# Optimization experiments

Hardware: AMD Instinct MI355X
Metric: run time of the kernel (lower is better)

The kernel has to match this reference:

```python
import jax, jax.numpy as jnp
import numpy as np

EPS = 1e-5

def setup_inputs() -> dict:
    key = jax.random.key(0)
    ks = jax.random.split(key, 12)
    N, d0, d1, d2, qh, qo = 8192, 128, 256, 256, 128, 1
    state = jax.random.normal(ks[0], (N, d0), dtype=jnp.float32)
    adjacent_matrix = jax.random.uniform(ks[1], (N, N), dtype=jnp.float32)
    s = 0.05
    return {
        "state": state,
        "adjacent_matrix": adjacent_matrix,
        "gamma": jnp.ones((d0,), jnp.float32),
        "beta": jnp.zeros((d0,), jnp.float32),
        "W1": jax.random.normal(ks[2], (d0, d1), jnp.float32) * s,
        "b1": jnp.zeros((d1,), jnp.float32),
        "W2": jax.random.normal(ks[3], (d1, d2), jnp.float32) * s,
        "b2": jnp.zeros((d2,), jnp.float32),
        "Wq1": jax.random.normal(ks[4], (d2, qh), jnp.float32) * s,
        "bq1": jnp.zeros((qh,), jnp.float32),
        "Wq2": jax.random.normal(ks[5], (qh, qo), jnp.float32) * s,
        "bq2": jnp.zeros((qo,), jnp.float32),
    }


def reference(state, adjacent_matrix, gamma, beta, W1, b1, W2, b2, Wq1, bq1, Wq2, bq2):
    # LinkBatchNorm: BatchNorm1d over node (batch) axis, training-mode statistics
    mean = jnp.mean(state, axis=0)
    var = jnp.var(state, axis=0)
    x = (state - mean) * jax.lax.rsqrt(var + EPS) * gamma + beta  # [N, d0]
    # GraphCNN: two layers of relu(A @ X @ W + b)
    h = jax.nn.relu(adjacent_matrix @ (x @ W1) + b1)   # [N, d1]
    h = jax.nn.relu(adjacent_matrix @ (h @ W2) + b2)   # [N, d2]
    # QNetwork: per-node MLP -> Q value
    q = jax.nn.relu(h @ Wq1 + bq1) @ Wq2 + bq2         # [N, 1]
    return q
```

## Files before the change

kernel.cpp:

```cpp
#include <hip/hip_runtime.h>
#include <stdint.h>

#define NN 8192
#define D0 128
#define D1 256
#define D2 256
#define QH 128
#define EPSV 1e-5f

using bf16x8 = __attribute__((ext_vector_type(8))) __bf16;
using f32x4  = __attribute__((ext_vector_type(4))) float;

__device__ __forceinline__ unsigned short f2bf(float f) {
    union { float f; unsigned int u; } v; v.f = f;
    unsigned int r = v.u + 0x7FFFu + ((v.u >> 16) & 1u);
    return (unsigned short)(r >> 16);
}
__device__ __forceinline__ float bf2f(unsigned short h) {
    union { unsigned int u; float f; } v; v.u = ((unsigned int)h) << 16;
    return v.f;
}
__device__ __forceinline__ void async_ld16(const void* g, void* l) {
    __builtin_amdgcn_global_load_lds(
        (__attribute__((address_space(1))) void*)(g),
        (__attribute__((address_space(3))) void*)(l), 16, 0, 0);
}

__global__ __launch_bounds__(256) void k_castA(const float* __restrict__ A,
                                               unsigned short* __restrict__ Abf,
                                               float* __restrict__ rs) {
    __shared__ float sred[256];
    int t = threadIdx.x;
    size_t row = blockIdx.x;
    const float* ap = A + row * NN;
    unsigned short* op = Abf + row * NN;
    float s = 0.f;
#pragma unroll
    for (int i = 0; i < 8; ++i) {
        int c = i * 1024 + t * 4;
        float4 v = *(const float4*)(ap + c);
        s += v.x + v.y + v.z + v.w;
        ushort4 o; o.x = f2bf(v.x); o.y = f2bf(v.y); o.z = f2bf(v.z); o.w = f2bf(v.w);
        *(ushort4*)(op + c) = o;
    }
    sred[t] = s;
    __syncthreads();
    if (t < 128) sred[t] += sred[t + 128];
    __syncthreads();
    if (t < 64) {
        float v = sred[t] + sred[t + 64];
#pragma unroll
        for (int d = 32; d > 0; d >>= 1) v += __shfl_down(v, d, 64);
        if (t == 0) rs[row] = v;
    }
}

__global__ void k_zero(float* __restrict__ p) {
    p[blockIdx.x * 256 + threadIdx.x] = 0.f;
}

__global__ void k_stats(const float* __restrict__ state,
                        float* __restrict__ psum, float* __restrict__ psq) {
    int j = threadIdx.x;
    int b = blockIdx.x;
    const float* p = state + (size_t)b * 32 * D0 + j;
    float s = 0.f, sq = 0.f;
#pragma unroll 4
    for (int r = 0; r < 32; ++r) { float x = p[(size_t)r * D0]; s += x; sq += x * x; }
    psum[b * D0 + j] = s;
    psq [b * D0 + j] = sq;
}

__global__ void k_finalize(const float* __restrict__ psum, const float* __restrict__ psq,
                           const float* __restrict__ gamma, const float* __restrict__ beta,
                           const float* __restrict__ W1,
                           float* __restrict__ scale, float* __restrict__ shift,
                           float* __restrict__ c1) {
    __shared__ float s_shift[D0];
    int t = threadIdx.x;
    if (t < D0) {
        float s = 0.f, sq = 0.f;
        for (int b = 0; b < 256; ++b) { s += psum[b * D0 + t]; sq += psq[b * D0 + t]; }
        float mean = s * (1.0f / NN);
        float var  = sq * (1.0f / NN) - mean * mean;
        float sc = gamma[t] * rsqrtf(var + EPSV);
        float sh = beta[t] - mean * sc;
        scale[t] = sc; shift[t] = sh; s_shift[t] = sh;
    }
    __syncthreads();
    float acc = 0.f;
    for (int k = 0; k < D0; ++k) acc += s_shift[k] * W1[(size_t)k * D1 + t];
    c1[t] = acc;
}

__global__ void k_prep_weights(const float* __restrict__ W1, const float* __restrict__ W2,
                               const float* __restrict__ scale,
                               unsigned short* __restrict__ W1st,
                               unsigned short* __restrict__ W2t) {
    int idx = blockIdx.x * 256 + threadIdx.x;
    if (idx < 32768) {
        int n = idx >> 7, k = idx & 127;
        W1st[idx] = f2bf(W1[(size_t)k * D1 + n] * scale[k]);
    } else {
        int i = idx - 32768; int n = i >> 8, k = i & 255;
        W2t[i] = f2bf(W2[(size_t)k * D2 + n]);
    }
}

template <int N, int K, bool A_FP32, bool BIAS>
__global__ __launch_bounds__(256, 4) void k_small_gemm(
        const void* __restrict__ Aptr, const unsigned short* __restrict__ Bt,
        const float* __restrict__ bias, unsigned short* __restrict__ out) {
    constexpr int WN = N / 4;
    constexpr int NJ = WN / 16;
    constexpr int BI = N / 64;
    __shared__ unsigned short Alds[32 * 32];
    __shared__ unsigned short Blds[N * 32];
    int t = threadIdx.x, lane = t & 63, w = t >> 6;
    int m0 = blockIdx.x * 32;
    int lr = lane & 15, lk = (lane >> 4) * 8;
    int wc = w * WN;
    f32x4 acc[2][NJ] = {};

    for (int kk = 0; kk < K; kk += 32) {
        __syncthreads();
        if constexpr (A_FP32) {
            const float* A = (const float*)Aptr;
            int row = t >> 3, kc = (t & 7) * 4;
            float4 v = *(const float4*)(A + (size_t)(m0 + row) * K + kk + kc);
            uint2 p;
            p.x = ((unsigned)f2bf(v.y) << 16) | f2bf(v.x);
            p.y = ((unsigned)f2bf(v.w) << 16) | f2bf(v.z);
            *(uint2*)&Alds[row * 32 + kc] = p;
        } else {
            if (w < 2) {
                const unsigned short* A = (const unsigned short*)Aptr;
                int row = w * 16 + (lane >> 2);
                async_ld16(A + (size_t)(m0 + row) * K + kk + (lane & 3) * 8, &Alds[w * 512]);
            }
        }
#pragma unroll
        for (int i = 0; i < BI; ++i) {
            int n = w * WN + i * 16 + (lane >> 2);
            async_ld16(Bt + (size_t)n * K + kk + (lane & 3) * 8, &Blds[(w * WN + i * 16) * 32]);
        }
        __syncthreads();
        bf16x8 a[2], b[NJ];
#pragma unroll
        for (int i = 0; i < 2; ++i) a[i] = *(const bf16x8*)&Alds[(i * 16 + lr) * 32 + lk];
#pragma unroll
        for (int j = 0; j < NJ; ++j) b[j] = *(const bf16x8*)&Blds[(wc + j * 16 + lr) * 32 + lk];
#pragma unroll
        for (int i = 0; i < 2; ++i)
#pragma unroll
            for (int j = 0; j < NJ; ++j)
                acc[i][j] = __builtin_amdgcn_mfma_f32_16x16x32_bf16(a[i], b[j], acc[i][j], 0, 0, 0);
    }
    int q = lane >> 4;
#pragma unroll
    for (int j = 0; j < NJ; ++j) {
        int n = wc + j * 16 + lr;
        float bv = 0.f;
        if constexpr (BIAS) bv = bias[n];
#pragma unroll
        for (int i = 0; i < 2; ++i) {
#pragma unroll
            for (int r = 0; r < 4; ++r) {
                int m = m0 + i * 16 + q * 4 + r;
                out[(size_t)m * N + n] = f2bf(acc[i][j][r] + bv);
            }
        }
    }
}

__global__ void k_transpose(const unsigned short* __restrict__ in, unsigned short* __restrict__ out,
                            float* __restrict__ colsum) {
    __shared__ unsigned short tile[64 * 68];
    __shared__ float cp[4][64];
    int t = threadIdx.x;
    int r0 = blockIdx.x * 64, c0 = blockIdx.y * 64;
#pragma unroll
    for (int p = 0; p < 4; ++p) {
        int row = (t >> 4) + p * 16, col = (t & 15) * 4;
        *(ushort4*)&tile[row * 68 + col] = *(const ushort4*)&in[(size_t)(r0 + row) * 256 + c0 + col];
    }
    __syncthreads();
    int n = t >> 2;
#pragma unroll
    for (int s = 0; s < 2; ++s) {
        int mo = (t & 3) * 16 + s * 8;
        unsigned short v[8];
#pragma unroll
        for (int e = 0; e < 8; ++e) v[e] = tile[(mo + e) * 68 + n];
        *(uint4*)&out[(size_t)(c0 + n) * NN + r0 + mo] = *(const uint4*)v;
    }
    int col = t & 63, gg = t >> 6;
    float s = 0.f;
#pragma unroll
    for (int r = 0; r < 16; ++r) s += bf2f(tile[(gg * 16 + r) * 68 + col]);
    cp[gg][col] = s;
    __syncthreads();
    if (t < 64) atomicAdd(colsum + c0 + t, cp[0][t] + cp[1][t] + cp[2][t] + cp[3][t]);
}

__global__ __launch_bounds__(512, 4) void k_big_gemm2(
        const unsigned short* __restrict__ Abf, const unsigned short* __restrict__ Yt,
        float* __restrict__ Cp) {
    __shared__ unsigned short Alds[128 * 32];
    __shared__ unsigned short Blds[256 * 32];
    int t = threadIdx.x, lane = t & 63, w = t >> 6;
    int m0 = blockIdx.x * 128;
    int kbeg = blockIdx.y * 1024;
    int wr = (w & 1) * 64, wc = (w >> 1) * 64;
    int lr = lane & 15, q = lane >> 4;
    f32x4 acc[4][4] = {};

    int srow = lane >> 2;
    int hsw = (lane & 3) ^ ((srow ^ (srow >> 2)) & 3);
    const unsigned short* agp = Abf + (size_t)(m0 + w * 16 + srow) * NN + kbeg + hsw * 8;
    const unsigned short* bg0 = Yt + (size_t)(w * 32 + srow) * NN + kbeg + hsw * 8;
    const unsigned short* bg1 = Yt + (size_t)(w * 32 + 16 + srow) * NN + kbeg + hsw * 8;
    unsigned short* aLb = Alds + w * 512;
    unsigned short* bLb0 = Blds + w * 1024;
    unsigned short* bLb1 = Blds + w * 1024 + 512;
    int xsr = (lr ^ (lr >> 2)) & 3;
    int lks = ((q ^ xsr) & 3) * 8;

    for (int kk = 0; kk < 1024; kk += 32) {
        __syncthreads();
        async_ld16(agp + kk, aLb);
        async_ld16(bg0 + kk, bLb0);
        async_ld16(bg1 + kk, bLb1);
        __syncthreads();
        bf16x8 a[4], b[4];
#pragma unroll
        for (int i = 0; i < 4; ++i) a[i] = *(const bf16x8*)&Alds[(wr + i * 16 + lr) * 32 + lks];
#pragma unroll
        for (int j = 0; j < 4; ++j) b[j] = *(const bf16x8*)&Blds[(wc + j * 16 + lr) * 32 + lks];
#pragma unroll
        for (int i = 0; i < 4; ++i)
#pragma unroll
            for (int j = 0; j < 4; ++j)
                acc[i][j] = __builtin_amdgcn_mfma_f32_16x16x32_bf16(a[i], b[j], acc[i][j], 0, 0, 0);
    }
    float* outp = Cp + (size_t)blockIdx.y * NN * 256;
#pragma unroll
    for (int i = 0; i < 4; ++i)
#pragma unroll
        for (int j = 0; j < 4; ++j) {
            int n = wc + j * 16 + lr;
#pragma unroll
            for (int r = 0; r < 4; ++r) {
                int m = m0 + wr + i * 16 + q * 4 + r;
                outp[(size_t)m * 256 + n] = acc[i][j][r];
            }
        }
}

__global__ void k_s2(const float* __restrict__ colB, const float* __restrict__ colH1,
                     const float* __restrict__ W2, float* __restrict__ s2) {
    int n = threadIdx.x;
    float acc = 0.f;
    for (int k = 0; k < 256; ++k) acc += colH1[k] * W2[(size_t)k * 256 + n];
    s2[n] = colB[n] - acc;
}

__global__ __launch_bounds__(256) void k_reduce8(
        const float* __restrict__ Cp, const float* __restrict__ rsA,
        const float* __restrict__ bias, const float* __restrict__ sn,
        unsigned short* __restrict__ out, float* __restrict__ colH1) {
    __shared__ float rs_s[16];
    __shared__ float cs[4][256];
    int t = threadIdx.x;
    int m0 = blockIdx.x * 16;
    const size_t S = (size_t)NN * 256;
    if (t < 16) rs_s[t] = rsA[m0 + t] * (1.0f / 8192.0f);
    __syncthreads();
    int g = t >> 6, cq = (t & 63) * 4;
    float4 snv = *(const float4*)(sn + cq);
    float4 bv  = *(const float4*)(bias + cq);
    float c0 = 0.f, c1a = 0.f, c2 = 0.f, c3 = 0.f;
#pragma unroll
    for (int r4 = 0; r4 < 4; ++r4) {
        int row = g * 4 + r4;
        size_t base = (size_t)(m0 + row) * 256 + cq;
        float4 a = {0.f, 0.f, 0.f, 0.f};
#pragma unroll
        for (int s = 0; s < 8; ++s) {
            float4 p = *(const float4*)(Cp + (size_t)s * S + base);
            a.x += p.x; a.y += p.y; a.z += p.z; a.w += p.w;
        }
        float rsv = rs_s[row];
        float x0 = fmaxf(a.x + bv.x - rsv * snv.x, 0.f);
        float x1 = fmaxf(a.y + bv.y - rsv * snv.y, 0.f);
        float x2 = fmaxf(a.z + bv.z - rsv * snv.z, 0.f);
        float x3 = fmaxf(a.w + bv.w - rsv * snv.w, 0.f);
        ushort4 o; o.x = f2bf(x0); o.y = f2bf(x1); o.z = f2bf(x2); o.w = f2bf(x3);
        *(ushort4*)(out + base) = o;
        c0 += x0; c1a += x1; c2 += x2; c3 += x3;
    }
    cs[g][cq] = c0; cs[g][cq + 1] = c1a; cs[g][cq + 2] = c2; cs[g][cq + 3] = c3;
    __syncthreads();
    float tot = cs[0][t] + cs[1][t] + cs[2][t] + cs[3][t];
    atomicAdd(colH1 + t, tot);
}

__global__ __launch_bounds__(256) void k_reduce_qhead(
        const float* __restrict__ Cp, const float* __restrict__ rsA,
        const float* __restrict__ bias, const float* __restrict__ sn,
        const float* __restrict__ Wq1, const float* __restrict__ bq1,
        const float* __restrict__ Wq2, const float* __restrict__ bq2,
        float* __restrict__ out) {
    __shared__ float sh[16][256];
    __shared__ float rs_s[16];
    __shared__ float red[4][8];
    int t = threadIdx.x;
    int m0 = blockIdx.x * 16;
    const size_t S = (size_t)NN * 256;
    if (t < 16) rs_s[t] = rsA[m0 + t] * (1.0f / 8192.0f);
    __syncthreads();
    int g = t >> 6, cq = (t & 63) * 4;
    float4 snv = *(const float4*)(sn + cq);
    float4 bv  = *(const float4*)(bias + cq);
#pragma unroll
    for (int r4 = 0; r4 < 4; ++r4) {
        int row = g * 4 + r4;
        size_t base = (size_t)(m0 + row) * 256 + cq;
        float4 a = {0.f, 0.f, 0.f, 0.f};
#pragma unroll
        for (int s = 0; s < 8; ++s) {
            float4 p = *(const float4*)(Cp + (size_t)s * S + base);
            a.x += p.x; a.y += p.y; a.z += p.z; a.w += p.w;
        }
        float rsv = rs_s[row];
        float4 o;
        o.x = fmaxf(a.x + bv.x - rsv * snv.x, 0.f);
        o.y = fmaxf(a.y + bv.y - rsv * snv.y, 0.f);
        o.z = fmaxf(a.z + bv.z - rsv * snv.z, 0.f);
        o.w = fmaxf(a.w + bv.w - rsv * snv.w, 0.f);
        *(float4*)&sh[row][cq] = o;
    }
    __syncthreads();
    int h = t & 127, rg = t >> 7;
    float acc[8] = {};
    for (int n = 0; n < 256; ++n) {
        float wv = Wq1[(size_t)n * QH + h];
#pragma unroll
        for (int r = 0; r < 8; ++r) acc[r] = fmaf(sh[rg * 8 + r][n], wv, acc[r]);
    }
    float b1v = bq1[h], w2v = Wq2[h];
    int wid = t >> 6, lane = t & 63;
#pragma unroll
    for (int r = 0; r < 8; ++r) {
        float v = fmaxf(acc[r] + b1v, 0.f) * w2v;
#pragma unroll
        for (int d = 32; d > 0; d >>= 1) v += __shfl_down(v, d, 64);
        if (lane == 0) red[wid][r] = v;
    }
    __syncthreads();
    if (t < 16) {
        int rg2 = t >> 3, r = t & 7;
        out[m0 + rg2 * 8 + r] = red[rg2 * 2][r] + red[rg2 * 2 + 1][r] + bq2[0];
    }
}

extern "C" void kernel_launch(void* const* d_in, const int* in_sizes, int n_in,
                              void* d_out, int out_size, void* d_ws, size_t ws_size,
                              hipStream_t stream) {
    const float* state = (const float*)d_in[0];
    const float* adj   = (const float*)d_in[1];
    const float* gamma = (const float*)d_in[2];
    const float* beta  = (const float*)d_in[3];
    const float* W1    = (const float*)d_in[4];
    const float* b1    = (const float*)d_in[5];
    const float* W2    = (const float*)d_in[6];
    const float* b2    = (const float*)d_in[7];
    const float* Wq1   = (const float*)d_in[8];
    const float* bq1   = (const float*)d_in[9];
    const float* Wq2   = (const float*)d_in[10];
    const float* bq2   = (const float*)d_in[11];
    float* out = (float*)d_out;

    char* ws = (char*)d_ws;
    float* psum  = (float*)(ws + 0);
    float* psq   = (float*)(ws + 131072);
    float* scale = (float*)(ws + 262144);
    float* shift = (float*)(ws + 262656);
    float* c1    = (float*)(ws + 263168);
    float* colA  = (float*)(ws + 264192);
    float* colB  = (float*)(ws + 265216);
    float* colH1 = (float*)(ws + 266240);
    float* s2    = (float*)(ws + 267264);
    unsigned short* W1st = (unsigned short*)(ws + 268288);
    unsigned short* W2t  = (unsigned short*)(ws + 333824);
    unsigned short* Ybuf = (unsigned short*)(ws + (size_t)1  * (1u << 20));
    unsigned short* Ytb  = (unsigned short*)(ws + (size_t)5  * (1u << 20));
    unsigned short* Hbuf = (unsigned short*)(ws + (size_t)9  * (1u << 20));
    float*          rsA  = (float*)(ws + (size_t)14 * (1u << 20));
    float*          Cp   = (float*)(ws + (size_t)22 * (1u << 20));
    unsigned short* Abf  = (unsigned short*)(ws + (size_t)128 * (1u << 20));

    k_castA<<<8192, 256, 0, stream>>>(adj, Abf, rsA);
    k_zero<<<4, 256, 0, stream>>>(colA);
    k_stats<<<256, 128, 0, stream>>>(state, psum, psq);
    k_finalize<<<1, 256, 0, stream>>>(psum, psq, gamma, beta, W1, scale, shift, c1);
    k_prep_weights<<<384, 256, 0, stream>>>(W1, W2, scale, W1st, W2t);

    k_small_gemm<256, 128, true, true><<<256, 256, 0, stream>>>(state, W1st, c1, Ybuf);
    k_transpose<<<dim3(128, 4), 256, 0, stream>>>(Ybuf, Ytb, colA);
    k_big_gemm2<<<dim3(64, 8), 512, 0, stream>>>(Abf, Ytb, Cp);
    k_reduce8<<<512, 256, 0, stream>>>(Cp, rsA, b1, colA, Hbuf, colH1);

    k_small_gemm<256, 256, false, false><<<256, 256, 0, stream>>>(Hbuf, W2t, nullptr, Ybuf);
    k_transpose<<<dim3(128, 4), 256, 0, stream>>>(Ybuf, Ytb, colB);
    k_s2<<<1, 256, 0, stream>>>(colB, colH1, W2, s2);
    k_big_gemm2<<<dim3(64, 8), 512, 0, stream>>>(Abf, Ytb, Cp);
    k_reduce_qhead<<<512, 256, 0, stream>>>(Cp, rsA, b2, s2, Wq1, bq1, Wq2, bq2, out);
}
```

Before: 608.1 us.

## Fuse fp32-to-bf16 cast of adjacency into first big GEMM, bf16 partials

Removes the separate k_castA pass. The first split-K GEMM now reads fp32 adjacency directly, converts it to bf16 into LDS, writes the bf16 copy out for reuse by the second GEMM, and accumulates per-split row sums. The GEMM tile is also reshaped to 64x256 with 256 threads, and the first GEMM's split-K partials are stored as bf16 to halve the partial-sum traffic. k_zero is folded into k_stats. The trade-offs are that synchronous A loads stall the MFMA loop and bf16 partials lose some precision.

```diff
diff --git a/kernel.cpp b/kernel.cpp
--- a/kernel.cpp
+++ b/kernel.cpp
@@ -26,43 +26,15 @@
         (__attribute__((address_space(3))) void*)(l), 16, 0, 0);
 }
 
-__global__ __launch_bounds__(256) void k_castA(const float* __restrict__ A,
-                                               unsigned short* __restrict__ Abf,
-                                               float* __restrict__ rs) {
-    __shared__ float sred[256];
-    int t = threadIdx.x;
-    size_t row = blockIdx.x;
-    const float* ap = A + row * NN;
-    unsigned short* op = Abf + row * NN;
-    float s = 0.f;
-#pragma unroll
-    for (int i = 0; i < 8; ++i) {
-        int c = i * 1024 + t * 4;
-        float4 v = *(const float4*)(ap + c);
-        s += v.x + v.y + v.z + v.w;
-        ushort4 o; o.x = f2bf(v.x); o.y = f2bf(v.y); o.z = f2bf(v.z); o.w = f2bf(v.w);
-        *(ushort4*)(op + c) = o;
-    }
-    sred[t] = s;
-    __syncthreads();
-    if (t < 128) sred[t] += sred[t + 128];
-    __syncthreads();
-    if (t < 64) {
-        float v = sred[t] + sred[t + 64];
-#pragma unroll
-        for (int d = 32; d > 0; d >>= 1) v += __shfl_down(v, d, 64);
-        if (t == 0) rs[row] = v;
-    }
-}
-
-__global__ void k_zero(float* __restrict__ p) {
-    p[blockIdx.x * 256 + threadIdx.x] = 0.f;
-}
-
 __global__ void k_stats(const float* __restrict__ state,
-                        float* __restrict__ psum, float* __restrict__ psq) {
+                        float* __restrict__ psum, float* __restrict__ psq,
+                        float* __restrict__ zero4k) {
     int j = threadIdx.x;
     int b = blockIdx.x;
+    if (b == 0) {
+#pragma unroll
+        for (int i = 0; i < 8; ++i) zero4k[i * 128 + j] = 0.f;
+    }
     const float* p = state + (size_t)b * 32 * D0 + j;
     float s = 0.f, sq = 0.f;
 #pragma unroll 4
@@ -203,38 +175,56 @@
     if (t < 64) atomicAdd(colsum + c0 + t, cp[0][t] + cp[1][t] + cp[2][t] + cp[3][t]);
 }
 
-__global__ __launch_bounds__(512, 4) void k_big_gemm2(
-        const unsigned short* __restrict__ Abf, const unsigned short* __restrict__ Yt,
-        float* __restrict__ Cp) {
-    __shared__ unsigned short Alds[128 * 32];
+template <bool CONVERT_A, bool CP_BF16>
+__global__ __launch_bounds__(256, 4) void k_big_gemm3(
+        const float* __restrict__ Af32, const unsigned short* __restrict__ Abf_in,
+        unsigned short* __restrict__ Abf_out, const unsigned short* __restrict__ Yt,
+        void* __restrict__ Cpv, float* __restrict__ rsPart) {
+    __shared__ unsigned short Alds[64 * 32];
     __shared__ unsigned short Blds[256 * 32];
     int t = threadIdx.x, lane = t & 63, w = t >> 6;
-    int m0 = blockIdx.x * 128;
+    int m0 = blockIdx.x * 64;
     int kbeg = blockIdx.y * 1024;
-    int wr = (w & 1) * 64, wc = (w >> 1) * 64;
+    int wc = w * 64;
     int lr = lane & 15, q = lane >> 4;
     f32x4 acc[4][4] = {};
 
     int srow = lane >> 2;
-    int hsw = (lane & 3) ^ ((srow ^ (srow >> 2)) & 3);
-    const unsigned short* agp = Abf + (size_t)(m0 + w * 16 + srow) * NN + kbeg + hsw * 8;
-    const unsigned short* bg0 = Yt + (size_t)(w * 32 + srow) * NN + kbeg + hsw * 8;
-    const unsigned short* bg1 = Yt + (size_t)(w * 32 + 16 + srow) * NN + kbeg + hsw * 8;
-    unsigned short* aLb = Alds + w * 512;
-    unsigned short* bLb0 = Blds + w * 1024;
-    unsigned short* bLb1 = Blds + w * 1024 + 512;
-    int xsr = (lr ^ (lr >> 2)) & 3;
-    int lks = ((q ^ xsr) & 3) * 8;
+    int hsw = (lane & 3) ^ ((srow >> 1) & 3);
+    const unsigned short* bg = Yt + (size_t)(w * 64 + srow) * NN + kbeg + hsw * 8;
+    unsigned short* bLb = Blds + (w * 64) * 32;
+    int arow = t >> 2, ac = t & 3;
+    int ah = ac ^ ((arow >> 1) & 3);
+    const float* agf = Af32 + (size_t)(m0 + arow) * NN + kbeg + ah * 8;
+    unsigned short* aof = Abf_out + (size_t)(m0 + arow) * NN + kbeg + ah * 8;
+    const unsigned short* agb = Abf_in + (size_t)(m0 + w * 16 + srow) * NN + kbeg + hsw * 8;
+    unsigned short* aLb = Alds + (w * 16) * 32;
+    int lks = ((q ^ ((lr >> 1) & 3)) & 3) * 8;
+    float rs = 0.f;
 
     for (int kk = 0; kk < 1024; kk += 32) {
         __syncthreads();
-        async_ld16(agp + kk, aLb);
-        async_ld16(bg0 + kk, bLb0);
-        async_ld16(bg1 + kk, bLb1);
+        if constexpr (CONVERT_A) {
+            float4 v0 = *(const float4*)(agf + kk);
+            float4 v1 = *(const float4*)(agf + kk + 4);
+            rs += v0.x + v0.y + v0.z + v0.w + v1.x + v1.y + v1.z + v1.w;
+            uint4 p;
+            p.x = ((unsigned)f2bf(v0.y) << 16) | f2bf(v0.x);
+            p.y = ((unsigned)f2bf(v0.w) << 16) | f2bf(v0.z);
+            p.z = ((unsigned)f2bf(v1.y) << 16) | f2bf(v1.x);
+            p.w = ((unsigned)f2bf(v1.w) << 16) | f2bf(v1.z);
+            *(uint4*)&Alds[arow * 32 + ac * 8] = p;
+            *(uint4*)(aof + kk) = p;
+        } else {
+            async_ld16(agb + kk, aLb);
+        }
+#pragma unroll
+        for (int g = 0; g < 4; ++g)
+            async_ld16(bg + (size_t)(g * 16) * NN + kk, bLb + (g * 16) * 32);
         __syncthreads();
         bf16x8 a[4], b[4];
 #pragma unroll
-        for (int i = 0; i < 4; ++i) a[i] = *(const bf16x8*)&Alds[(wr + i * 16 + lr) * 32 + lks];
+        for (int i = 0; i < 4; ++i) a[i] = *(const bf16x8*)&Alds[(i * 16 + lr) * 32 + lks];
 #pragma unroll
         for (int j = 0; j < 4; ++j) b[j] = *(const bf16x8*)&Blds[(wc + j * 16 + lr) * 32 + lks];
 #pragma unroll
@@ -243,18 +233,34 @@
             for (int j = 0; j < 4; ++j)
                 acc[i][j] = __builtin_amdgcn_mfma_f32_16x16x32_bf16(a[i], b[j], acc[i][j], 0, 0, 0);
     }
-    float* outp = Cp + (size_t)blockIdx.y * NN * 256;
-#pragma unroll
-    for (int i = 0; i < 4; ++i)
-#pragma unroll
-        for (int j = 0; j < 4; ++j) {
-            int n = wc + j * 16 + lr;
-#pragma unroll
-            for (int r = 0; r < 4; ++r) {
-                int m = m0 + wr + i * 16 + q * 4 + r;
-                outp[(size_t)m * 256 + n] = acc[i][j][r];
+    if constexpr (CONVERT_A) {
+        rs += __shfl_xor(rs, 1, 64);
+        rs += __shfl_xor(rs, 2, 64);
+        if (ac == 0) rsPart[(size_t)blockIdx.y * NN + m0 + arow] = rs;
+    }
+    if constexpr (CP_BF16) {
+        unsigned short* outp = (unsigned short*)Cpv + (size_t)blockIdx.y * NN * 256;
+#pragma unroll
+        for (int i = 0; i < 4; ++i)
+#pragma unroll
+            for (int j = 0; j < 4; ++j) {
+                int n = wc + j * 16 + lr;
+#pragma unroll
+                for (int r = 0; r < 4; ++r)
+                    outp[(size_t)(m0 + i * 16 + q * 4 + r) * 256 + n] = f2bf(acc[i][j][r]);
             }
-        }
+    } else {
+        float* outp = (float*)Cpv + (size_t)blockIdx.y * NN * 256;
+#pragma unroll
+        for (int i = 0; i < 4; ++i)
+#pragma unroll
+            for (int j = 0; j < 4; ++j) {
+                int n = wc + j * 16 + lr;
+#pragma unroll
+                for (int r = 0; r < 4; ++r)
+                    outp[(size_t)(m0 + i * 16 + q * 4 + r) * 256 + n] = acc[i][j][r];
+            }
+    }
 }
 
 __global__ void k_s2(const float* __restrict__ colB, const float* __restrict__ colH1,
@@ -266,15 +272,21 @@
 }
 
 __global__ __launch_bounds__(256) void k_reduce8(
-        const float* __restrict__ Cp, const float* __restrict__ rsA,
-        const float* __restrict__ bias, const float* __restrict__ sn,
+        const unsigned short* __restrict__ Cp, const float* __restrict__ rsPart,
+        float* __restrict__ rsA, const float* __restrict__ bias, const float* __restrict__ sn,
         unsigned short* __restrict__ out, float* __restrict__ colH1) {
     __shared__ float rs_s[16];
     __shared__ float cs[4][256];
     int t = threadIdx.x;
     int m0 = blockIdx.x * 16;
     const size_t S = (size_t)NN * 256;
-    if (t < 16) rs_s[t] = rsA[m0 + t] * (1.0f / 8192.0f);
+    if (t < 16) {
+        float r = 0.f;
+#pragma unroll
+        for (int s = 0; s < 8; ++s) r += rsPart[(size_t)s * NN + m0 + t];
+        rsA[m0 + t] = r;
+        rs_s[t] = r * (1.0f / 8192.0f);
+    }
     __syncthreads();
     int g = t >> 6, cq = (t & 63) * 4;
     float4 snv = *(const float4*)(sn + cq);
@@ -284,17 +296,17 @@
     for (int r4 = 0; r4 < 4; ++r4) {
         int row = g * 4 + r4;
         size_t base = (size_t)(m0 + row) * 256 + cq;
-        float4 a = {0.f, 0.f, 0.f, 0.f};
+        float a0 = 0.f, a1 = 0.f, a2 = 0.f, a3 = 0.f;
 #pragma unroll
         for (int s = 0; s < 8; ++s) {
-            float4 p = *(const float4*)(Cp + (size_t)s * S + base);
-            a.x += p.x; a.y += p.y; a.z += p.z; a.w += p.w;
+            ushort4 p = *(const ushort4*)(Cp + (size_t)s * S + base);
+            a0 += bf2f(p.x); a1 += bf2f(p.y); a2 += bf2f(p.z); a3 += bf2f(p.w);
         }
         float rsv = rs_s[row];
-        float x0 = fmaxf(a.x + bv.x - rsv * snv.x, 0.f);
-        float x1 = fmaxf(a.y + bv.y - rsv * snv.y, 0.f);
-        float x2 = fmaxf(a.z + bv.z - rsv * snv.z, 0.f);
-        float x3 = fmaxf(a.w + bv.w - rsv * snv.w, 0.f);
+        float x0 = fmaxf(a0 + bv.x - rsv * snv.x, 0.f);
+        float x1 = fmaxf(a1 + bv.y - rsv * snv.y, 0.f);
+        float x2 = fmaxf(a2 + bv.z - rsv * snv.z, 0.f);
+        float x3 = fmaxf(a3 + bv.w - rsv * snv.w, 0.f);
         ushort4 o; o.x = f2bf(x0); o.y = f2bf(x1); o.z = f2bf(x2); o.w = f2bf(x3);
         *(ushort4*)(out + base) = o;
         c0 += x0; c1a += x1; c2 += x2; c3 += x3;
@@ -396,24 +408,23 @@
     unsigned short* Ybuf = (unsigned short*)(ws + (size_t)1  * (1u << 20));
     unsigned short* Ytb  = (unsigned short*)(ws + (size_t)5  * (1u << 20));
     unsigned short* Hbuf = (unsigned short*)(ws + (size_t)9  * (1u << 20));
-    float*          rsA  = (float*)(ws + (size_t)14 * (1u << 20));
-    float*          Cp   = (float*)(ws + (size_t)22 * (1u << 20));
+    float*          rsP  = (float*)(ws + (size_t)14 * (1u << 20));
+    float*          rsA  = (float*)(ws + (size_t)15 * (1u << 20));
+    void*           Cp   = (void*)(ws + (size_t)22 * (1u << 20));
     unsigned short* Abf  = (unsigned short*)(ws + (size_t)128 * (1u << 20));
 
-    k_castA<<<8192, 256, 0, stream>>>(adj, Abf, rsA);
-    k_zero<<<4, 256, 0, stream>>>(colA);
-    k_stats<<<256, 128, 0, stream>>>(state, psum, psq);
+    k_stats<<<256, 128, 0, stream>>>(state, psum, psq, colA);
     k_finalize<<<1, 256, 0, stream>>>(psum, psq, gamma, beta, W1, scale, shift, c1);
     k_prep_weights<<<384, 256, 0, stream>>>(W1, W2, scale, W1st, W2t);
 
     k_small_gemm<256, 128, true, true><<<256, 256, 0, stream>>>(state, W1st, c1, Ybuf);
     k_transpose<<<dim3(128, 4), 256, 0, stream>>>(Ybuf, Ytb, colA);
-    k_big_gemm2<<<dim3(64, 8), 512, 0, stream>>>(Abf, Ytb, Cp);
-    k_reduce8<<<512, 256, 0, stream>>>(Cp, rsA, b1, colA, Hbuf, colH1);
+    k_big_gemm3<true, true><<<dim3(128, 8), 256, 0, stream>>>(adj, nullptr, Abf, Ytb, Cp, rsP);
+    k_reduce8<<<512, 256, 0, stream>>>((const unsigned short*)Cp, rsP, rsA, b1, colA, Hbuf, colH1);
 
     k_small_gemm<256, 256, false, false><<<256, 256, 0, stream>>>(Hbuf, W2t, nullptr, Ybuf);
     k_transpose<<<dim3(128, 4), 256, 0, stream>>>(Ybuf, Ytb, colB);
     k_s2<<<1, 256, 0, stream>>>(colB, colH1, W2, s2);
-    k_big_gemm2<<<dim3(64, 8), 512, 0, stream>>>(Abf, Ytb, Cp);
-    k_reduce_qhead<<<512, 256, 0, stream>>>(Cp, rsA, b2, s2, Wq1, bq1, Wq2, bq2, out);
-}
+    k_big_gemm3<false, false><<<dim3(128, 8), 256, 0, stream>>>(nullptr, Abf, nullptr, Ytb, Cp, nullptr);
+    k_reduce_qhead<<<512, 256, 0, stream>>>((const float*)Cp, rsA, b2, s2, Wq1, bq1, Wq2, bq2, out);
+}
```

New measurement: 653.9 us. +7.5%, slower.
